# Performance work log

Hardware: AMD Instinct MI355X
Metric: run time of the kernel (lower is better)

The kernel has to match this reference:

```python
import jax, jax.numpy as jnp
import numpy as np

NEG_INF_SCALE = -1e9


def setup_inputs() -> dict:
    key = jax.random.key(0)
    ks = jax.random.split(key, 8)
    B, T, M, D = 64, 1024, 256, 1024
    query = jax.random.normal(ks[0], (B, 1, M), dtype=jnp.float32)
    keys = jax.random.normal(ks[1], (B, T, M), dtype=jnp.float32)
    values = jax.random.normal(ks[2], (B, T, D), dtype=jnp.float32)
    mask = jax.random.randint(ks[3], (B, 1, T), 0, 2).astype(jnp.float32)
    # MLP params (scaled like torch default init ~ 1/sqrt(fan_in))
    W1 = jax.random.normal(ks[4], (4 * M, D), dtype=jnp.float32) / np.sqrt(4 * M)
    b1 = jnp.zeros((D,), dtype=jnp.float32)
    W2 = jax.random.normal(ks[5], (D, D), dtype=jnp.float32) / np.sqrt(D)
    b2 = jnp.zeros((D,), dtype=jnp.float32)
    w_score = jax.random.normal(ks[6], (D, 1), dtype=jnp.float32) / np.sqrt(D)
    b_score = jnp.zeros((1,), dtype=jnp.float32)
    return {"query": query, "keys": keys, "values": values, "mask": mask,
            "W1": W1, "b1": b1, "W2": W2, "b2": b2,
            "w_score": w_score, "b_score": b_score}


def reference(query, keys, values, mask, W1, b1, W2, b2, w_score, b_score):
    # query: [B,1,M] broadcast against keys: [B,T,M]
    q = jnp.broadcast_to(query, keys.shape)
    att_input = jnp.concatenate([q, keys, q - keys, q * keys], axis=-1)  # [B,T,4M]
    h = jax.nn.relu(att_input @ W1 + b1)   # [B,T,D]
    h = jax.nn.relu(h @ W2 + b2)           # [B,T,D]
    score = h @ w_score + b_score          # [B,T,1]
    logits = jnp.swapaxes(score, 1, 2)     # [B,1,T]
    logits = logits + mask * NEG_INF_SCALE
    attn = jax.nn.softmax(logits, axis=-1)  # [B,1,T]
    out = jnp.matmul(attn, values)          # [B,1,D]
    return out
```

## Files before the change

### kernel.cpp

```cpp
#include <hip/hip_runtime.h>

#define DEV __device__ __forceinline__

typedef __attribute__((ext_vector_type(4))) float f32x4;
typedef __attribute__((ext_vector_type(8))) short short8;
typedef __attribute__((ext_vector_type(4))) short s16x4;
typedef __attribute__((ext_vector_type(4))) float f32x4v;

DEV short f2bf(float f) {
  union { float f; unsigned u; } v; v.f = f;
  unsigned r = (v.u + 0x7FFFu + ((v.u >> 16) & 1u)) >> 16;
  return (short)r;
}

DEV void gload16(const void* g, void* l) {
  __builtin_amdgcn_global_load_lds(
      (const __attribute__((address_space(1))) void*)g,
      (__attribute__((address_space(3))) void*)l, 16, 0, 0);
}

#define BAR() __builtin_amdgcn_s_barrier()
#define LGKMW(n)                                              \
  {                                                           \
    asm volatile("s_waitcnt lgkmcnt(" #n ")" ::: "memory");   \
    __builtin_amdgcn_sched_barrier(0);                        \
  }
#define VMW(n)                                                \
  {                                                           \
    asm volatile("s_waitcnt vmcnt(" #n ")" ::: "memory");     \
    __builtin_amdgcn_sched_barrier(0);                        \
  }


__global__ __launch_bounds__(256) void k_prep_keys(const float* __restrict__ k,
                                                   short* __restrict__ o) {
  int i = (blockIdx.x * 256 + threadIdx.x) * 8;
  f32x4v v0 = *(const f32x4v*)(k + i);
  f32x4v v1 = *(const f32x4v*)(k + i + 4);
  short8 s;
  s[0] = f2bf(v0[0]); s[1] = f2bf(v0[1]); s[2] = f2bf(v0[2]); s[3] = f2bf(v0[3]);
  s[4] = f2bf(v1[0]); s[5] = f2bf(v1[1]); s[6] = f2bf(v1[2]); s[7] = f2bf(v1[3]);
  *(short8*)(o + i) = s;
}

__global__ __launch_bounds__(256) void k_prep_w2t(const float* __restrict__ w2,
                                                  short* __restrict__ w2t) {
  __shared__ float tile[64][65];
  const int k0 = blockIdx.x * 64, n0 = blockIdx.y * 64;
  const int a = threadIdx.x & 63, q = threadIdx.x >> 6;
#pragma unroll
  for (int i = 0; i < 16; ++i) {
    int kk = i * 4 + q;
    tile[kk][a] = w2[(size_t)(k0 + kk) * 1024 + n0 + a];
  }
  __syncthreads();
#pragma unroll
  for (int i = 0; i < 16; ++i) {
    int nn = i * 4 + q;
    w2t[(size_t)(n0 + nn) * 1024 + k0 + a] = f2bf(tile[a][nn]);
  }
}

__global__ __launch_bounds__(256) void k_prep_wkt(const float* __restrict__ w1,
                                                  const float* __restrict__ query,
                                                  const float* __restrict__ b1,
                                                  short* __restrict__ wkt,
                                                  float* __restrict__ biasb) {
  __shared__ short tile[64][257];
  __shared__ float redm[64][4];
  const int b = blockIdx.x, d0 = blockIdx.y * 64;
  const int d = threadIdx.x & 63, mq = threadIdx.x >> 6;
  float bacc = 0.f;
#pragma unroll 4
  for (int i = 0; i < 64; ++i) {
    int m = i * 4 + mq;
    float qv = query[b * 256 + m];
    float wa = w1[(size_t)m * 1024 + d0 + d];
    float wb = w1[(size_t)(256 + m) * 1024 + d0 + d];
    float wc = w1[(size_t)(512 + m) * 1024 + d0 + d];
    float wd = w1[(size_t)(768 + m) * 1024 + d0 + d];
    tile[d][m] = f2bf(wb - wc + qv * wd);
    bacc += qv * (wa + wc);
  }
  redm[d][mq] = bacc;
  __syncthreads();
  const int m = threadIdx.x;
  for (int dd = 0; dd < 64; ++dd)
    wkt[((size_t)b * 1024 + d0 + dd) * 256 + m] = tile[dd][m];
  if (threadIdx.x < 64) {
    int dd = threadIdx.x;
    biasb[b * 1024 + d0 + dd] =
        redm[dd][0] + redm[dd][1] + redm[dd][2] + redm[dd][3] + b1[d0 + dd];
  }
}


template <int MODE>
__global__ __launch_bounds__(256, 2) void k_gemm(const short* __restrict__ A,
                                                 const short* __restrict__ B,
                                                 const float* __restrict__ bias,
                                                 const float* __restrict__ wscore,
                                                 short* __restrict__ hout,
                                                 float* __restrict__ spart) {
  __shared__ short lds[24576];
  constexpr int SK = (MODE == 1) ? 256 : 1024;
  constexpr int KT = (MODE == 1) ? 8 : 32;

  const int tid = threadIdx.x;
  const int bx = blockIdx.x;
  const int L = (bx & 7) * 256 + (bx >> 3);

  const short *Ab, *Bb;
  const float *biasp, *wsp = nullptr;
  short* houtp = nullptr;
  int rt, ct;
  if constexpr (MODE == 1) {
    const int b = L >> 5;
    rt = (L >> 2) & 7; ct = L & 3;
    Ab = A + ((size_t)b * 1024 + rt * 128) * 256;
    Bb = B + ((size_t)b * 1024 + ct * 256) * 256;
    biasp = bias + b * 1024 + ct * 256;
    houtp = hout + ((size_t)(b * 1024 + rt * 128)) * 1024 + ct * 256;
  } else {
    rt = L >> 2; ct = L & 3;
    Ab = A + (size_t)rt * 128 * 1024;
    Bb = B + (size_t)ct * 256 * 1024;
    biasp = bias + ct * 256;
    wsp = wscore + ct * 256;
  }

  int gA[2], dA[2], gB[4], dB[4];
#pragma unroll
  for (int j = 0; j < 2; ++j) {
    int s = tid + j * 256, row = s >> 2, c = (s & 3) ^ ((row >> 1) & 3);
    gA[j] = row * SK + c * 8;
    dA[j] = s * 8;
  }
#pragma unroll
  for (int j = 0; j < 4; ++j) {
    int s = tid + j * 256, row = s >> 2, c = (s & 3) ^ ((row >> 1) & 3);
    gB[j] = row * SK + c * 8;
    dB[j] = 4096 + s * 8;
  }

  auto STAGE = [&](int kt, int buf) {
#pragma unroll
    for (int j = 0; j < 2; ++j) gload16(Ab + gA[j] + kt * 32, &lds[buf + dA[j]]);
#pragma unroll
    for (int j = 0; j < 4; ++j) gload16(Bb + gB[j] + kt * 32, &lds[buf + dB[j]]);
  };

  const int lane = tid & 63, l15 = lane & 15, l4 = lane >> 4, wc = tid >> 6;
  const int swz = (l4 ^ ((l15 >> 1) & 3)) * 8;
  const int aoff = l15 * 32 + swz;
  const int boff = 4096 + wc * 512 + l15 * 32 + swz;

  f32x4 acc[8][4];
#pragma unroll
  for (int m = 0; m < 8; ++m)
#pragma unroll
    for (int n = 0; n < 4; ++n) acc[m][n] = f32x4{0.f, 0.f, 0.f, 0.f};

  STAGE(0, 0);
#pragma unroll 2
  for (int kt = 0; kt < KT; ++kt) {
    const int cur = (kt & 1) * 12288;
    if (kt + 1 < KT) {
      STAGE(kt + 1, 12288 - cur);
      VMW(6);
    } else {
      VMW(0);
    }
    BAR();
    short8 af[8], bf[4];
#pragma unroll
    for (int m = 0; m < 8; ++m) af[m] = *(const short8*)&lds[cur + aoff + m * 512];
#pragma unroll
    for (int n = 0; n < 4; ++n) bf[n] = *(const short8*)&lds[cur + boff + n * 2048];
    LGKMW(0);
    BAR();
    __builtin_amdgcn_s_setprio(1);
#pragma unroll
    for (int m = 0; m < 8; ++m)
#pragma unroll
      for (int n = 0; n < 4; ++n)
        acc[m][n] = __builtin_amdgcn_mfma_f32_16x16x32_bf16(bf[n], af[m],
                                                            acc[m][n], 0, 0, 0);
    __builtin_amdgcn_s_setprio(0);
  }

  if constexpr (MODE == 1) {
    float bv[4][4];
#pragma unroll
    for (int n = 0; n < 4; ++n)
#pragma unroll
      for (int r2 = 0; r2 < 4; ++r2)
        bv[n][r2] = biasp[n * 64 + wc * 16 + l4 * 4 + r2];
#pragma unroll
    for (int m = 0; m < 8; ++m) {
      int row = m * 16 + l15;
#pragma unroll
      for (int n = 0; n < 4; ++n) {
        s16x4 pk;
#pragma unroll
        for (int r2 = 0; r2 < 4; ++r2)
          pk[r2] = f2bf(fmaxf(acc[m][n][r2] + bv[n][r2], 0.f));
        *(s16x4*)&houtp[(size_t)row * 1024 + n * 64 + wc * 16 + l4 * 4] = pk;
      }
    }
  } else {
    float bv[4][4], wv[4][4];
#pragma unroll
    for (int n = 0; n < 4; ++n)
#pragma unroll
      for (int r2 = 0; r2 < 4; ++r2) {
        int c = n * 64 + wc * 16 + l4 * 4 + r2;
        bv[n][r2] = biasp[c];
        wv[n][r2] = wsp[c];
      }
    float* so = spart + ((size_t)(ct * 4 + wc) << 16) + rt * 128;
#pragma unroll
    for (int m = 0; m < 8; ++m) {
      float s = 0.f;
#pragma unroll
      for (int n = 0; n < 4; ++n)
#pragma unroll
        for (int r2 = 0; r2 < 4; ++r2)
          s += fmaxf(acc[m][n][r2] + bv[n][r2], 0.f) * wv[n][r2];
      s += __shfl_xor(s, 16);
      s += __shfl_xor(s, 32);
      if (lane < 16) so[m * 16 + l15] = s;
    }
  }
}


__global__ __launch_bounds__(256) void k_softmax(const float* __restrict__ spart,
                                                 const float* __restrict__ mask,
                                                 const float* __restrict__ bscore,
                                                 float* __restrict__ attn) {
  const int b = blockIdx.x, tid = threadIdx.x;
  __shared__ float sm[1024];
  __shared__ float red[8];
  const float bs = bscore[0];
  float lmax = -3.0e38f;
  for (int t = tid; t < 1024; t += 256) {
    float s = bs;
#pragma unroll
    for (int c = 0; c < 16; ++c) s += spart[(size_t)c * 65536 + b * 1024 + t];
    float lg = s + mask[b * 1024 + t] * (-1e9f);
    sm[t] = lg;
    lmax = fmaxf(lmax, lg);
  }
  for (int o = 32; o; o >>= 1) lmax = fmaxf(lmax, __shfl_xor(lmax, o));
  const int wid = tid >> 6, lane = tid & 63;
  if (lane == 0) red[wid] = lmax;
  __syncthreads();
  float bmax = fmaxf(fmaxf(red[0], red[1]), fmaxf(red[2], red[3]));
  float lsum = 0.f;
  for (int t = tid; t < 1024; t += 256) {
    float e = __expf(sm[t] - bmax);
    sm[t] = e;
    lsum += e;
  }
  for (int o = 32; o; o >>= 1) lsum += __shfl_xor(lsum, o);
  __syncthreads();
  if (lane == 0) red[wid] = lsum;
  __syncthreads();
  float inv = 1.0f / (red[0] + red[1] + red[2] + red[3]);
  for (int t = tid; t < 1024; t += 256) attn[b * 1024 + t] = sm[t] * inv;
}

__global__ __launch_bounds__(256) void k_out(const float* __restrict__ attn,
                                             const float* __restrict__ values,
                                             float* __restrict__ part) {
  const int b = blockIdx.x >> 3, ts = blockIdx.x & 7;
  const int tid = threadIdx.x;
  __shared__ float at[128];
  if (tid < 128) at[tid] = attn[b * 1024 + ts * 128 + tid];
  __syncthreads();
  const float* vb = values + ((size_t)b * 1024 + ts * 128) * 1024 + tid * 4;
  f32x4 acc = {0.f, 0.f, 0.f, 0.f};
#pragma unroll 8
  for (int t = 0; t < 128; ++t) {
    f32x4v v = *(const f32x4v*)(vb + (size_t)t * 1024);
    float a = at[t];
    acc[0] += a * v[0]; acc[1] += a * v[1]; acc[2] += a * v[2]; acc[3] += a * v[3];
  }
  *(f32x4*)(part + ((size_t)(b * 8 + ts)) * 1024 + tid * 4) = acc;
}

__global__ __launch_bounds__(256) void k_red(const float* __restrict__ part,
                                             float* __restrict__ out) {
  const int b = blockIdx.x;
  const int c4 = threadIdx.x * 4;
  f32x4 s = {0.f, 0.f, 0.f, 0.f};
#pragma unroll
  for (int ts = 0; ts < 8; ++ts) {
    f32x4v v = *(const f32x4v*)(part + ((size_t)(b * 8 + ts)) * 1024 + c4);
    s[0] += v[0]; s[1] += v[1]; s[2] += v[2]; s[3] += v[3];
  }
  *(f32x4*)(out + b * 1024 + c4) = s;
}


extern "C" void kernel_launch(void* const* d_in, const int* in_sizes, int n_in,
                              void* d_out, int out_size, void* d_ws, size_t ws_size,
                              hipStream_t stream) {
  const float* query  = (const float*)d_in[0];
  const float* keys   = (const float*)d_in[1];
  const float* values = (const float*)d_in[2];
  const float* mask   = (const float*)d_in[3];
  const float* W1     = (const float*)d_in[4];
  const float* b1     = (const float*)d_in[5];
  const float* W2     = (const float*)d_in[6];
  const float* b2     = (const float*)d_in[7];
  const float* wscore = (const float*)d_in[8];
  const float* bscore = (const float*)d_in[9];
  float* out = (float*)d_out;

  char* ws = (char*)d_ws;
  short* keysb = (short*)(ws);
  short* wkt   = (short*)(ws + 33554432ull);
  short* w2t   = (short*)(ws + 67108864ull);
  float* biasb = (float*)(ws + 69206016ull);
  short* h1    = (short*)(ws + 69468160ull);
  float* spart = (float*)(ws + 203685888ull);
  float* attn  = (float*)(ws + 207880192ull);
  float* part  = (float*)(ws + 208142336ull);

  k_prep_keys<<<8192, 256, 0, stream>>>(keys, keysb);
  k_prep_w2t<<<dim3(16, 16), 256, 0, stream>>>(W2, w2t);
  k_prep_wkt<<<dim3(64, 16), 256, 0, stream>>>(W1, query, b1, wkt, biasb);

  k_gemm<1><<<2048, 256, 0, stream>>>(keysb, wkt, biasb, nullptr, h1, nullptr);
  k_gemm<2><<<2048, 256, 0, stream>>>(h1, w2t, b2, wscore, nullptr, spart);

  k_softmax<<<64, 256, 0, stream>>>(spart, mask, bscore, attn);
  k_out<<<512, 256, 0, stream>>>(attn, values, part);
  k_red<<<64, 256, 0, stream>>>(part, out);
}
```

Measured before the change: 293.3 us.

## Pre-swizzle weight operands into MFMA fragment layout and load B directly to registers

```diff
diff --git a/kernel.cpp b/kernel.cpp
--- a/kernel.cpp
+++ b/kernel.cpp
@@ -43,30 +43,34 @@
   *(short8*)(o + i) = s;
 }
 
-__global__ __launch_bounds__(256) void k_prep_w2t(const float* __restrict__ w2,
-                                                  short* __restrict__ w2t) {
+__global__ __launch_bounds__(256) void k_prep_w2f(const float* __restrict__ w2,
+                                                  short* __restrict__ w2f) {
   __shared__ float tile[64][65];
-  const int k0 = blockIdx.x * 64, n0 = blockIdx.y * 64;
+  const int kt = blockIdx.x, n0 = blockIdx.y * 64;
   const int a = threadIdx.x & 63, q = threadIdx.x >> 6;
 #pragma unroll
   for (int i = 0; i < 16; ++i) {
     int kk = i * 4 + q;
-    tile[kk][a] = w2[(size_t)(k0 + kk) * 1024 + n0 + a];
-  }
-  __syncthreads();
-#pragma unroll
-  for (int i = 0; i < 16; ++i) {
-    int nn = i * 4 + q;
-    w2t[(size_t)(n0 + nn) * 1024 + k0 + a] = f2bf(tile[a][nn]);
+    tile[kk][a] = w2[(size_t)(kt * 64 + kk) * 1024 + n0 + a];
+  }
+  __syncthreads();
+  const int l = threadIdx.x & 63, cgl = threadIdx.x >> 6;
+#pragma unroll
+  for (int kh = 0; kh < 2; ++kh) {
+    short8 v;
+#pragma unroll
+    for (int j = 0; j < 8; ++j)
+      v[j] = f2bf(tile[kh * 32 + (l >> 4) * 8 + j][cgl * 16 + (l & 15)]);
+    *(short8*)&w2f[((size_t)((kt * 2 + kh) * 64 + (n0 >> 4) + cgl)) * 512 + l * 8] = v;
   }
 }
 
 __global__ __launch_bounds__(256) void k_prep_wkt(const float* __restrict__ w1,
                                                   const float* __restrict__ query,
                                                   const float* __restrict__ b1,
-                                                  short* __restrict__ wkt,
+                                                  short* __restrict__ wktf,
                                                   float* __restrict__ biasb) {
-  __shared__ short tile[64][257];
+  __shared__ short tile[64][264];
   __shared__ float redm[64][4];
   const int b = blockIdx.x, d0 = blockIdx.y * 64;
   const int d = threadIdx.x & 63, mq = threadIdx.x >> 6;
@@ -84,9 +88,16 @@
   }
   redm[d][mq] = bacc;
   __syncthreads();
-  const int m = threadIdx.x;
-  for (int dd = 0; dd < 64; ++dd)
-    wkt[((size_t)b * 1024 + d0 + dd) * 256 + m] = tile[dd][m];
+  const int l = threadIdx.x & 63, cgl = threadIdx.x >> 6;
+  short* ob = wktf + (size_t)b * 262144;
+#pragma unroll
+  for (int kt = 0; kt < 4; ++kt)
+#pragma unroll
+    for (int kh = 0; kh < 2; ++kh) {
+      short8 v = *(const short8*)&tile[cgl * 16 + (l & 15)]
+                                      [kt * 64 + kh * 32 + (l >> 4) * 8];
+      *(short8*)&ob[((size_t)((kt * 2 + kh) * 64 + (d0 >> 4) + cgl)) * 512 + l * 8] = v;
+    }
   if (threadIdx.x < 64) {
     int dd = threadIdx.x;
     biasb[b * 1024 + d0 + dd] =
@@ -97,14 +108,14 @@
 
 template <int MODE>
 __global__ __launch_bounds__(256, 2) void k_gemm(const short* __restrict__ A,
-                                                 const short* __restrict__ B,
+                                                 const short* __restrict__ Bf,
                                                  const float* __restrict__ bias,
                                                  const float* __restrict__ wscore,
                                                  short* __restrict__ hout,
                                                  float* __restrict__ spart) {
-  __shared__ short lds[24576];
+  __shared__ short lds[32768];
   constexpr int SK = (MODE == 1) ? 256 : 1024;
-  constexpr int KT = (MODE == 1) ? 8 : 32;
+  constexpr int KT = (MODE == 1) ? 4 : 16;
 
   const int tid = threadIdx.x;
   const int bx = blockIdx.x;
@@ -117,77 +128,92 @@
   if constexpr (MODE == 1) {
     const int b = L >> 5;
     rt = (L >> 2) & 7; ct = L & 3;
-    Ab = A + ((size_t)b * 1024 + rt * 128) * 256;
-    Bb = B + ((size_t)b * 1024 + ct * 256) * 256;
+    Ab = A + ((size_t)(b * 1024 + rt * 128)) * 256;
+    Bb = Bf + (size_t)b * 262144;
     biasp = bias + b * 1024 + ct * 256;
     houtp = hout + ((size_t)(b * 1024 + rt * 128)) * 1024 + ct * 256;
   } else {
     rt = L >> 2; ct = L & 3;
     Ab = A + (size_t)rt * 128 * 1024;
-    Bb = B + (size_t)ct * 256 * 1024;
+    Bb = Bf;
     biasp = bias + ct * 256;
     wsp = wscore + ct * 256;
   }
 
-  int gA[2], dA[2], gB[4], dB[4];
-#pragma unroll
-  for (int j = 0; j < 2; ++j) {
-    int s = tid + j * 256, row = s >> 2, c = (s & 3) ^ ((row >> 1) & 3);
-    gA[j] = row * SK + c * 8;
+  int gA[4], dA[4];
+#pragma unroll
+  for (int j = 0; j < 4; ++j) {
+    int s = tid + j * 256, row = s >> 3, kc = (s & 7) ^ (row & 7);
+    gA[j] = row * SK + kc * 8;
     dA[j] = s * 8;
   }
-#pragma unroll
-  for (int j = 0; j < 4; ++j) {
-    int s = tid + j * 256, row = s >> 2, c = (s & 3) ^ ((row >> 1) & 3);
-    gB[j] = row * SK + c * 8;
-    dB[j] = 4096 + s * 8;
-  }
-
-  auto STAGE = [&](int kt, int buf) {
-#pragma unroll
-    for (int j = 0; j < 2; ++j) gload16(Ab + gA[j] + kt * 32, &lds[buf + dA[j]]);
-#pragma unroll
-    for (int j = 0; j < 4; ++j) gload16(Bb + gB[j] + kt * 32, &lds[buf + dB[j]]);
+  auto STAGE = [&](int kt) {
+    const int bb = (kt & 3) * 8192;
+#pragma unroll
+    for (int j = 0; j < 4; ++j) gload16(Ab + gA[j] + kt * 64, &lds[bb + dA[j]]);
   };
 
   const int lane = tid & 63, l15 = lane & 15, l4 = lane >> 4, wc = tid >> 6;
-  const int swz = (l4 ^ ((l15 >> 1) & 3)) * 8;
-  const int aoff = l15 * 32 + swz;
-  const int boff = 4096 + wc * 512 + l15 * 32 + swz;
+  const int afo0 = l15 * 64 + ((l4 ^ (l15 & 7)) * 8);
+  const int afo1 = l15 * 64 + (((4 + l4) ^ (l15 & 7)) * 8);
 
   f32x4 acc[8][4];
 #pragma unroll
   for (int m = 0; m < 8; ++m)
 #pragma unroll
     for (int n = 0; n < 4; ++n) acc[m][n] = f32x4{0.f, 0.f, 0.f, 0.f};
-
-  STAGE(0, 0);
-#pragma unroll 2
-  for (int kt = 0; kt < KT; ++kt) {
-    const int cur = (kt & 1) * 12288;
-    if (kt + 1 < KT) {
-      STAGE(kt + 1, 12288 - cur);
-      VMW(6);
+  short8 bf[2][4][2];
+  short8 af[8];
+
+#define LOADB(kt, BK_)                                                          \
+  _Pragma("unroll") for (int n_ = 0; n_ < 4; ++n_) {                            \
+    _Pragma("unroll") for (int kh_ = 0; kh_ < 2; ++kh_) {                       \
+      bf[BK_][n_][kh_] = *(const short8*)(Bb +                                  \
+          ((size_t)(((kt) * 2 + kh_) * 64 + ct * 16 + n_ * 4 + wc) << 9) +      \
+          lane * 8);                                                            \
+    }                                                                           \
+  }
+
+  STAGE(0); LOADB(0, 0);
+  STAGE(1); LOADB(1, 1);
+  VMW(12);
+  BAR();
+
+#pragma unroll
+  for (int t = 0; t < KT; ++t) {
+    const int bb = (t & 3) * 8192;
+#pragma unroll
+    for (int m = 0; m < 8; ++m) af[m] = *(const short8*)&lds[bb + afo0 + m * 1024];
+    LGKMW(0);
+    __builtin_amdgcn_s_setprio(1);
+#pragma unroll
+    for (int m = 0; m < 8; ++m)
+#pragma unroll
+      for (int n = 0; n < 4; ++n)
+        acc[m][n] = __builtin_amdgcn_mfma_f32_16x16x32_bf16(bf[t & 1][n][0], af[m],
+                                                            acc[m][n], 0, 0, 0);
+    __builtin_amdgcn_s_setprio(0);
+#pragma unroll
+    for (int m = 0; m < 8; ++m) af[m] = *(const short8*)&lds[bb + afo1 + m * 1024];
+    if (t + 2 < KT) STAGE(t + 2);
+    LGKMW(0);
+    __builtin_amdgcn_s_setprio(1);
+#pragma unroll
+    for (int m = 0; m < 8; ++m)
+#pragma unroll
+      for (int n = 0; n < 4; ++n)
+        acc[m][n] = __builtin_amdgcn_mfma_f32_16x16x32_bf16(bf[t & 1][n][1], af[m],
+                                                            acc[m][n], 0, 0, 0);
+    __builtin_amdgcn_s_setprio(0);
+    if (t + 2 < KT) {
+      LOADB(t + 2, (t & 1));
+      VMW(12);
     } else {
       VMW(0);
     }
     BAR();
-    short8 af[8], bf[4];
-#pragma unroll
-    for (int m = 0; m < 8; ++m) af[m] = *(const short8*)&lds[cur + aoff + m * 512];
-#pragma unroll
-    for (int n = 0; n < 4; ++n) bf[n] = *(const short8*)&lds[cur + boff + n * 2048];
-    LGKMW(0);
-    BAR();
-    __builtin_amdgcn_s_setprio(1);
-#pragma unroll
-    for (int m = 0; m < 8; ++m)
-#pragma unroll
-      for (int n = 0; n < 4; ++n)
-        acc[m][n] = __builtin_amdgcn_mfma_f32_16x16x32_bf16(bf[n], af[m],
-                                                            acc[m][n], 0, 0, 0);
-    __builtin_amdgcn_s_setprio(0);
-  }
+  }
+#undef LOADB
 
   if constexpr (MODE == 1) {
     float bv[4][4];
@@ -321,8 +347,8 @@
 
   char* ws = (char*)d_ws;
   short* keysb = (short*)(ws);
-  short* wkt   = (short*)(ws + 33554432ull);
-  short* w2t   = (short*)(ws + 67108864ull);
+  short* wktf  = (short*)(ws + 33554432ull);
+  short* w2f   = (short*)(ws + 67108864ull);
   float* biasb = (float*)(ws + 69206016ull);
   short* h1    = (short*)(ws + 69468160ull);
   float* spart = (float*)(ws + 203685888ull);
@@ -330,11 +356,11 @@
   float* part  = (float*)(ws + 208142336ull);
 
   k_prep_keys<<<8192, 256, 0, stream>>>(keys, keysb);
-  k_prep_w2t<<<dim3(16, 16), 256, 0, stream>>>(W2, w2t);
-  k_prep_wkt<<<dim3(64, 16), 256, 0, stream>>>(W1, query, b1, wkt, biasb);
-
-  k_gemm<1><<<2048, 256, 0, stream>>>(keysb, wkt, biasb, nullptr, h1, nullptr);
-  k_gemm<2><<<2048, 256, 0, stream>>>(h1, w2t, b2, wscore, nullptr, spart);
+  k_prep_w2f<<<dim3(16, 16), 256, 0, stream>>>(W2, w2f);
+  k_prep_wkt<<<dim3(64, 16), 256, 0, stream>>>(W1, query, b1, wktf, biasb);
+
+  k_gemm<1><<<2048, 256, 0, stream>>>(keysb, wktf, biasb, nullptr, h1, nullptr);
+  k_gemm<2><<<2048, 256, 0, stream>>>(h1, w2f, b2, wscore, nullptr, spart);
 
   k_softmax<<<64, 256, 0, stream>>>(spart, mask, bscore, attn);
   k_out<<<512, 256, 0, stream>>>(attn, values, part);
```

Measured after the change: 271.8 us. -7.3%, faster.
